# Optimization experiments

Measured on AMD Instinct MI355X. Metric: run time of the kernel, lower is better.

Reference implementation:

```python
import jax, jax.numpy as jnp
import numpy as np

EPS = 1e-10


def setup_inputs() -> dict:
    key = jax.random.key(0)
    k_in, k_len, k_u, k_w, k_b, k_cb = jax.random.split(key, 6)
    B, S, D_in = 16, 4096, 512
    G, C, D_out = 2, 320, 256
    inputs = jax.random.normal(k_in, (B, S, D_in), dtype=jnp.float32)
    valid_lengths = jax.random.randint(k_len, (B,), 1, S + 1, dtype=jnp.int64)
    noise_u = jax.random.uniform(k_u, (B, S, G, C), dtype=jnp.float32)
    # projector params (nn.Linear default init scale is irrelevant for correctness)
    W = jax.random.normal(k_w, (G * C, D_in), dtype=jnp.float32) * (1.0 / np.sqrt(D_in))
    b = jax.random.normal(k_b, (G * C,), dtype=jnp.float32) * 0.01
    codebook = jax.random.uniform(k_cb, (G, C, D_out // G), dtype=jnp.float32,
                                  minval=-1.0 / C, maxval=1.0 / C)
    temperature = jnp.asarray(2.0, dtype=jnp.float32)
    return {"inputs": inputs, "valid_lengths": valid_lengths, "noise_u": noise_u,
            "W": W, "b": b, "codebook": codebook, "temperature": temperature}


def reference(inputs, valid_lengths, noise_u, W, b, codebook, temperature):
    B, S, _ = inputs.shape
    G, C, Dg = codebook.shape
    # dense projector GEMM: [B,S,Din] @ [Din,G*C]
    logits = (jnp.einsum('bsi,oi->bso', inputs, W) + b).reshape(B, S, G, C)
    # gumbel-softmax with straight-through hard selection (F.gumbel_softmax)
    gumbels = -jnp.log(-jnp.log(noise_u + EPS) + EPS)
    y_soft = jax.nn.softmax((logits + gumbels) / temperature, axis=-1)
    idx = jnp.argmax(y_soft, axis=-1)                       # [B,S,G]
    y_hard = jax.nn.one_hot(idx, C, dtype=y_soft.dtype)
    choice_probs = y_hard - jax.lax.stop_gradient(y_soft) + y_soft
    # masked usage stats over valid positions
    soft_probs = jax.nn.softmax(logits, axis=-1)            # [B,S,G,C]
    mask = (jnp.arange(S)[None, :] < valid_lengths[:, None]).astype(soft_probs.dtype)
    masked_sum = jnp.einsum('bsgc,bs->gc', soft_probs, mask)
    usage = masked_sum / jnp.sum(mask)
    # per-group codebook lookup via einsum against small table
    quantized = jnp.einsum('bsgc,gcd->bsgd', choice_probs, codebook).reshape(B, S, G * Dg)
    return quantized, usage
```

## Files before the change

kernel.cpp:

```cpp
#include <hip/hip_runtime.h>
#include <math.h>

#define NB 16
#define NS 4096
#define DIN 512
#define NG 2
#define NC 320
#define GC 640
#define DG 128
#define NROW (NB*NS)
#define EPSV 1e-10f

typedef __attribute__((ext_vector_type(4))) float f32x4;
typedef __attribute__((ext_vector_type(8))) _Float16 f16x8;
typedef __attribute__((ext_vector_type(4))) _Float16 f16x4v;

__device__ __forceinline__ void gload_lds16(const void* g, void* l) {
    __builtin_amdgcn_global_load_lds(
        (const __attribute__((address_space(1))) void*)g,
        (__attribute__((address_space(3))) void*)l,
        16, 0, 0);
}

__global__ __launch_bounds__(256) void cvt_split(
    const float* __restrict__ src, _Float16* __restrict__ h,
    _Float16* __restrict__ l, int n4)
{
    int i = blockIdx.x * 256 + threadIdx.x;
    if (i >= n4) return;
    float4 v = ((const float4*)src)[i];
    f16x4v vh, vl;
    float xs[4] = {v.x, v.y, v.z, v.w};
    #pragma unroll
    for (int j = 0; j < 4; ++j) {
        _Float16 hh = (_Float16)xs[j];
        vh[j] = hh;
        vl[j] = (_Float16)((xs[j] - (float)hh) * 2048.0f);
    }
    ((f16x4v*)h)[i] = vh;
    ((f16x4v*)l)[i] = vl;
}

__global__ __launch_bounds__(256, 2) void mfma_logits(
    const _Float16* __restrict__ Xh, const _Float16* __restrict__ Xl,
    const _Float16* __restrict__ Wh, const _Float16* __restrict__ Wl,
    const float* __restrict__ bias, float* __restrict__ logits)
{
    __shared__ _Float16 sA[2][2][128 * 32];
    __shared__ _Float16 sB[2][2][128 * 32];

    const int t = threadIdx.x;
    const int lane = t & 63;
    const int w = t >> 6;
    const int wm = w >> 1, wn = w & 1;

    const int p = blockIdx.x;
    const int o = (p & 7) * 320 + (p >> 3);
    const int mb = o / 5, nb = o - mb * 5;
    const int row0 = mb * 128, n0 = nb * 128;

    const int rl = lane >> 2;
    const int sl = (lane & 3) ^ ((lane >> 3) & 3);

    auto stage = [&](int b, int k0) {
        #pragma unroll
        for (int j = 0; j < 2; ++j) {
            int i = 2 * w + j;
            int ro = 16 * i + rl;
            size_t ga = (size_t)(row0 + ro) * DIN + k0 + 8 * sl;
            size_t gb = (size_t)(n0 + ro) * DIN + k0 + 8 * sl;
            gload_lds16(Xh + ga, &sA[b][0][i * 512]);
            gload_lds16(Xl + ga, &sA[b][1][i * 512]);
            gload_lds16(Wh + gb, &sB[b][0][i * 512]);
            gload_lds16(Wl + gb, &sB[b][1][i * 512]);
        }
    };

    f32x4 accA[4][4], accB[4][4];
    const f32x4 zz = {0.f, 0.f, 0.f, 0.f};
    #pragma unroll
    for (int mt = 0; mt < 4; ++mt)
        #pragma unroll
        for (int nt = 0; nt < 4; ++nt) { accA[mt][nt] = zz; accB[mt][nt] = zz; }

    stage(0, 0);
    __syncthreads();

    for (int ks = 0; ks < 16; ++ks) {
        const int cur = ks & 1;
        if (ks < 15) stage(cur ^ 1, (ks + 1) * 32);

        f16x8 ah[4], al[4], bh[4], bl[4];
        #pragma unroll
        for (int mt = 0; mt < 4; ++mt) {
            int r = wm * 64 + mt * 16 + (lane & 15);
            int idx = r * 32 + 8 * ((lane >> 4) ^ ((r >> 1) & 3));
            ah[mt] = *(const f16x8*)&sA[cur][0][idx];
            al[mt] = *(const f16x8*)&sA[cur][1][idx];
        }
        #pragma unroll
        for (int nt = 0; nt < 4; ++nt) {
            int r = wn * 64 + nt * 16 + (lane & 15);
            int idx = r * 32 + 8 * ((lane >> 4) ^ ((r >> 1) & 3));
            bh[nt] = *(const f16x8*)&sB[cur][0][idx];
            bl[nt] = *(const f16x8*)&sB[cur][1][idx];
        }
        #pragma unroll
        for (int mt = 0; mt < 4; ++mt)
            #pragma unroll
            for (int nt = 0; nt < 4; ++nt) {
                accA[mt][nt] = __builtin_amdgcn_mfma_f32_16x16x32_f16(ah[mt], bh[nt], accA[mt][nt], 0, 0, 0);
                accB[mt][nt] = __builtin_amdgcn_mfma_f32_16x16x32_f16(ah[mt], bl[nt], accB[mt][nt], 0, 0, 0);
                accB[mt][nt] = __builtin_amdgcn_mfma_f32_16x16x32_f16(al[mt], bh[nt], accB[mt][nt], 0, 0, 0);
            }
        __syncthreads();
    }

    #pragma unroll
    for (int nt = 0; nt < 4; ++nt) {
        int col = n0 + wn * 64 + nt * 16 + (lane & 15);
        float bv = bias[col];
        #pragma unroll
        for (int mt = 0; mt < 4; ++mt) {
            #pragma unroll
            for (int q = 0; q < 4; ++q) {
                int row = row0 + wm * 64 + mt * 16 + (lane >> 4) * 4 + q;
                logits[(size_t)row * GC + col] =
                    accA[mt][nt][q] + accB[mt][nt][q] * (1.0f / 2048.0f) + bv;
            }
        }
    }
}

#define RTB 32
__global__ __launch_bounds__(256, 8) void epilogue(
    const float* __restrict__ logits, const int* __restrict__ vlen,
    const float* __restrict__ U, const float* __restrict__ CB,
    float* __restrict__ out, float* __restrict__ gacc)
{
    __shared__ float uacc[GC];
    const int t = threadIdx.x;
    const int lane = t & 63;
    const int wid = t >> 6;
    const int row0 = blockIdx.x * RTB;

    for (int i = t; i < GC; i += 256) uacc[i] = 0.0f;
    __syncthreads();

    const int vl = vlen[row0 >> 12];

    float ureg[10];
    #pragma unroll
    for (int j = 0; j < 10; ++j) ureg[j] = 0.0f;

    #pragma unroll
    for (int r = 0; r < 8; ++r) {
        const int row = row0 + wid * 8 + r;
        const bool valid = (row & (NS - 1)) < vl;

        float lg[10], zz[10];
        #pragma unroll
        for (int j = 0; j < 10; ++j)
            lg[j] = logits[(size_t)row * GC + lane + 64 * j];
        #pragma unroll
        for (int j = 0; j < 10; ++j) {
            float u = U[(size_t)row * GC + lane + 64 * j];
            zz[j] = lg[j] - logf(-logf(u + EPSV) + EPSV);
        }

        #pragma unroll
        for (int g = 0; g < 2; ++g) {
            const int j0 = g * 5;

            float mv = zz[j0];
            #pragma unroll
            for (int j = j0 + 1; j < j0 + 5; ++j) mv = fmaxf(mv, zz[j]);
            #pragma unroll
            for (int d = 1; d < 64; d <<= 1) mv = fmaxf(mv, __shfl_xor(mv, d));

            int c = 0;
            #pragma unroll
            for (int jj = 4; jj >= 0; --jj) {
                unsigned long long b = __ballot(zz[j0 + jj] == mv);
                if (b) c = (__ffsll(b) - 1) + 64 * jj;
            }

            float pe[5], s2 = 0.0f;
            #pragma unroll
            for (int jj = 0; jj < 5; ++jj) {
                pe[jj] = __expf(lg[j0 + jj]);
                s2 += pe[jj];
            }
            #pragma unroll
            for (int d = 1; d < 64; d <<= 1) s2 += __shfl_xor(s2, d);
            if (valid) {
                const float inv = 1.0f / s2;
                #pragma unroll
                for (int jj = 0; jj < 5; ++jj) ureg[j0 + jj] += pe[jj] * inv;
            }

            const float2 cv = ((const float2*)(CB + ((size_t)g * NC + c) * DG))[lane];
            ((float2*)(out + (size_t)row * (NG * DG) + g * DG))[lane] = cv;
        }
    }

    #pragma unroll
    for (int j = 0; j < 10; ++j)
        atomicAdd(&uacc[lane + 64 * j], ureg[j]);

    __syncthreads();
    for (int i = t; i < GC; i += 256) atomicAdd(&gacc[i], uacc[i]);
}

__global__ void finalize_usage(const float* __restrict__ gacc,
                               const int* __restrict__ vlen,
                               float* __restrict__ usage_out)
{
    int total = 0;
    #pragma unroll
    for (int b = 0; b < NB; ++b) total += vlen[b];
    int o = threadIdx.x;
    if (o < GC) usage_out[o] = gacc[o] / (float)total;
}

#define RT 32
#define KC 8
#define NIT (DIN/KC)

__global__ void transpose_w(const float* __restrict__ W, float* __restrict__ Wt) {
    int idx = blockIdx.x * 256 + threadIdx.x;
    if (idx >= GC * DIN) return;
    int k = idx / GC, o = idx - k * GC;
    Wt[idx] = W[(size_t)o * DIN + k];
}

__global__ __launch_bounds__(256, 2) void fused_main(
    const float* __restrict__ X, const int* __restrict__ vlen,
    const float* __restrict__ U, const float* __restrict__ Wt,
    const float* __restrict__ bias, const float* __restrict__ CB,
    const float* __restrict__ tptr, float* __restrict__ out,
    float* __restrict__ gacc)
{
    __shared__ __align__(16) float WtC[2][KC][GC];
    __shared__ __align__(16) float AC[2][RT][KC];
    __shared__ float uacc[GC];

    const int t = threadIdx.x;
    const int lane = t & 63;
    const int wid = t >> 6;
    const int row0 = blockIdx.x * RT;

    for (int i = t; i < GC; i += 256) uacc[i] = 0.0f;

    float acc[8][10];
    #pragma unroll
    for (int r = 0; r < 8; ++r)
        #pragma unroll
        for (int j = 0; j < 10; ++j) acc[r][j] = 0.0f;

    auto stage = [&](int b, int k0) {
        const float* gw = Wt + (size_t)k0 * GC;
        #pragma unroll
        for (int i = 0; i < 5; ++i) {
            int base = (wid * 5 + i) * 256;
            gload_lds16(gw + base + 4 * lane, &WtC[b][0][0] + base);
        }
        if (wid == 0) {
            const float* gx = X + (size_t)(row0 + (lane >> 1)) * DIN + k0 + 4 * (lane & 1);
            gload_lds16(gx, &AC[b][0][0]);
        }
    };

    stage(0, 0);
    __syncthreads();

    int cur = 0;
    for (int it = 0; it < NIT; ++it) {
        if (it + 1 < NIT) stage(cur ^ 1, (it + 1) * KC);
        #pragma unroll
        for (int kk = 0; kk < KC; ++kk) {
            float w[10];
            #pragma unroll
            for (int j = 0; j < 10; ++j) w[j] = WtC[cur][kk][lane + 64 * j];
            #pragma unroll
            for (int r = 0; r < 8; ++r) {
                float a = AC[cur][wid * 8 + r][kk];
                #pragma unroll
                for (int j = 0; j < 10; ++j) acc[r][j] = fmaf(a, w[j], acc[r][j]);
            }
        }
        __syncthreads();
        cur ^= 1;
    }

    float bv[10];
    #pragma unroll
    for (int j = 0; j < 10; ++j) bv[j] = bias[lane + 64 * j];
    #pragma unroll
    for (int r = 0; r < 8; ++r)
        #pragma unroll
        for (int j = 0; j < 10; ++j) acc[r][j] += bv[j];

    const float T = *tptr;
    const int vl = vlen[row0 >> 12];

    #pragma unroll
    for (int r = 0; r < 8; ++r) {
        const int row = row0 + wid * 8 + r;
        const int ss = row & (NS - 1);
        const bool valid = ss < vl;

        float z[10];
        #pragma unroll
        for (int j = 0; j < 10; ++j) {
            float u = U[(size_t)row * GC + lane + 64 * j];
            float gn = -logf(-logf(u + EPSV) + EPSV);
            z[j] = (acc[r][j] + gn) / T;
        }

        #pragma unroll
        for (int g = 0; g < 2; ++g) {
            const int j0 = g * 5;
            float mv = z[j0];
            int mo = lane + 64 * j0;
            #pragma unroll
            for (int j = j0 + 1; j < j0 + 5; ++j) {
                if (z[j] > mv) { mv = z[j]; mo = lane + 64 * j; }
            }
            #pragma unroll
            for (int d = 1; d < 64; d <<= 1) {
                float ov = __shfl_xor(mv, d);
                int   oo = __shfl_xor(mo, d);
                if (ov > mv || (ov == mv && oo < mo)) { mv = ov; mo = oo; }
            }
            float se = 0.0f;
            #pragma unroll
            for (int j = j0; j < j0 + 5; ++j) se += expf(z[j] - mv);
            #pragma unroll
            for (int d = 1; d < 64; d <<= 1) se += __shfl_xor(se, d);
            float y = 1.0f / se;
            float q = (1.0f - y) + y;

            float m2 = acc[r][j0];
            #pragma unroll
            for (int j = j0 + 1; j < j0 + 5; ++j) m2 = fmaxf(m2, acc[r][j]);
            #pragma unroll
            for (int d = 1; d < 64; d <<= 1) m2 = fmaxf(m2, __shfl_xor(m2, d));
            float pe[5];
            float s2 = 0.0f;
            #pragma unroll
            for (int jj = 0; jj < 5; ++jj) {
                pe[jj] = expf(acc[r][j0 + jj] - m2);
                s2 += pe[jj];
            }
            #pragma unroll
            for (int d = 1; d < 64; d <<= 1) s2 += __shfl_xor(s2, d);
            if (valid) {
                #pragma unroll
                for (int jj = 0; jj < 5; ++jj)
                    atomicAdd(&uacc[lane + 64 * (j0 + jj)], pe[jj] / s2);
            }

            const int c = mo - g * NC;
            const float2 cv = ((const float2*)(CB + ((size_t)g * NC + c) * DG))[lane];
            float2 ov2;
            ov2.x = q * cv.x;
            ov2.y = q * cv.y;
            ((float2*)(out + (size_t)row * (NG * DG) + g * DG))[lane] = ov2;
        }
    }

    __syncthreads();
    for (int i = t; i < GC; i += 256) atomicAdd(&gacc[i], uacc[i]);
}

extern "C" void kernel_launch(void* const* d_in, const int* in_sizes, int n_in,
                              void* d_out, int out_size, void* d_ws, size_t ws_size,
                              hipStream_t stream)
{
    const float* X    = (const float*)d_in[0];
    const int*   vlen = (const int*)d_in[1];
    const float* U    = (const float*)d_in[2];
    const float* W    = (const float*)d_in[3];
    const float* bias = (const float*)d_in[4];
    const float* CB   = (const float*)d_in[5];
    const float* T    = (const float*)d_in[6];
    float* out = (float*)d_out;

    char* ws = (char*)d_ws;
    float*     Wt   = (float*)ws;
    float*     gacc = (float*)(ws + 1310720);
    _Float16*  Whh  = (_Float16*)(ws + 1313792);
    _Float16*  Wll  = (_Float16*)(ws + 1969152);
    _Float16*  Xhh  = (_Float16*)(ws + 2624512);
    _Float16*  Xll  = (_Float16*)(ws + 69733376);
    float*     lgts = (float*)(ws + 136842240);
    const size_t need = 136842240ull + 167772160ull;

    hipMemsetAsync(gacc, 0, GC * sizeof(float), stream);

    if (ws_size >= need) {
        const int nx4 = NROW * DIN / 4;
        const int nw4 = GC * DIN / 4;
        cvt_split<<<(nx4 + 255) / 256, 256, 0, stream>>>(X, Xhh, Xll, nx4);
        cvt_split<<<(nw4 + 255) / 256, 256, 0, stream>>>(W, Whh, Wll, nw4);
        mfma_logits<<<(NROW / 128) * 5, 256, 0, stream>>>(Xhh, Xll, Whh, Wll, bias, lgts);
        epilogue<<<NROW / RTB, 256, 0, stream>>>(lgts, vlen, U, CB, out, gacc);
    } else {
        transpose_w<<<(GC * DIN + 255) / 256, 256, 0, stream>>>(W, Wt);
        fused_main<<<NROW / RT, 256, 0, stream>>>(X, vlen, U, Wt, bias, CB, T, out, gacc);
    }
    finalize_usage<<<1, GC, 0, stream>>>(gacc, vlen, out + (size_t)NROW * (NG * DG));
}
```

Measured before the change: 333.0 us.

## Fuse fp32-to-fp16 split of X into GEMM A-tile staging

Drops the separate cvt_split pass over the large input X. The GEMM kernel now loads fp32 X directly into registers, splits each value into high and low fp16 parts, and writes them to LDS after the MFMAs, overlapping with the next tile's loads. This avoids writing and re-reading two fp16 copies of X, about 128 MB of extra traffic. It also moves to 512-thread blocks with 8 waves, each wave covering a 64x32 output sub-tile, which cuts per-thread accumulator registers. The cost is that the conversion work and register-staged loads now sit inside the GEMM main loop.

```diff
diff --git a/kernel.cpp b/kernel.cpp
--- a/kernel.cpp
+++ b/kernel.cpp
@@ -41,8 +41,8 @@
     ((f16x4v*)l)[i] = vl;
 }
 
-__global__ __launch_bounds__(256, 2) void mfma_logits(
-    const _Float16* __restrict__ Xh, const _Float16* __restrict__ Xl,
+__global__ __launch_bounds__(512, 3) void mfma_logits2(
+    const float* __restrict__ X,
     const _Float16* __restrict__ Wh, const _Float16* __restrict__ Wl,
     const float* __restrict__ bias, float* __restrict__ logits)
 {
@@ -52,7 +52,7 @@
     const int t = threadIdx.x;
     const int lane = t & 63;
     const int w = t >> 6;
-    const int wm = w >> 1, wn = w & 1;
+    const int wm = w >> 2, wn = w & 3;
 
     const int p = blockIdx.x;
     const int o = (p & 7) * 320 + (p >> 3);
@@ -62,35 +62,52 @@
     const int rl = lane >> 2;
     const int sl = (lane & 3) ^ ((lane >> 3) & 3);
 
-    auto stage = [&](int b, int k0) {
-        #pragma unroll
-        for (int j = 0; j < 2; ++j) {
-            int i = 2 * w + j;
-            int ro = 16 * i + rl;
-            size_t ga = (size_t)(row0 + ro) * DIN + k0 + 8 * sl;
-            size_t gb = (size_t)(n0 + ro) * DIN + k0 + 8 * sl;
-            gload_lds16(Xh + ga, &sA[b][0][i * 512]);
-            gload_lds16(Xl + ga, &sA[b][1][i * 512]);
-            gload_lds16(Wh + gb, &sB[b][0][i * 512]);
-            gload_lds16(Wl + gb, &sB[b][1][i * 512]);
-        }
+    auto stageB = [&](int b, int k0) {
+        int ro = 16 * w + rl;
+        size_t gb = (size_t)(n0 + ro) * DIN + k0 + 8 * sl;
+        gload_lds16(Wh + gb, &sB[b][0][w * 512]);
+        gload_lds16(Wl + gb, &sB[b][1][w * 512]);
     };
 
-    f32x4 accA[4][4], accB[4][4];
+    const int ar = t >> 2, aq = t & 3;
+    const int aidx = ar * 32 + 8 * (aq ^ ((ar >> 1) & 3));
+    const float* aga = X + (size_t)(row0 + ar) * DIN + 8 * aq;
+
+    float4 a0, a1;
+    auto loadA = [&](int k0) {
+        a0 = ((const float4*)(aga + k0))[0];
+        a1 = ((const float4*)(aga + k0))[1];
+    };
+    auto writeA = [&](int b) {
+        float xs[8] = {a0.x, a0.y, a0.z, a0.w, a1.x, a1.y, a1.z, a1.w};
+        f16x8 h, l;
+        #pragma unroll
+        for (int j = 0; j < 8; ++j) {
+            _Float16 hh = (_Float16)xs[j];
+            h[j] = hh;
+            l[j] = (_Float16)((xs[j] - (float)hh) * 2048.0f);
+        }
+        *(f16x8*)&sA[b][0][aidx] = h;
+        *(f16x8*)&sA[b][1][aidx] = l;
+    };
+
+    f32x4 accA[4][2], accB[4][2];
     const f32x4 zz = {0.f, 0.f, 0.f, 0.f};
     #pragma unroll
     for (int mt = 0; mt < 4; ++mt)
         #pragma unroll
-        for (int nt = 0; nt < 4; ++nt) { accA[mt][nt] = zz; accB[mt][nt] = zz; }
-
-    stage(0, 0);
+        for (int nt = 0; nt < 2; ++nt) { accA[mt][nt] = zz; accB[mt][nt] = zz; }
+
+    loadA(0);
+    stageB(0, 0);
+    writeA(0);
     __syncthreads();
 
     for (int ks = 0; ks < 16; ++ks) {
         const int cur = ks & 1;
-        if (ks < 15) stage(cur ^ 1, (ks + 1) * 32);
-
-        f16x8 ah[4], al[4], bh[4], bl[4];
+        if (ks < 15) { loadA((ks + 1) * 32); stageB(cur ^ 1, (ks + 1) * 32); }
+
+        f16x8 ah[4], al[4], bh[2], bl[2];
         #pragma unroll
         for (int mt = 0; mt < 4; ++mt) {
             int r = wm * 64 + mt * 16 + (lane & 15);
@@ -99,8 +116,8 @@
             al[mt] = *(const f16x8*)&sA[cur][1][idx];
         }
         #pragma unroll
-        for (int nt = 0; nt < 4; ++nt) {
-            int r = wn * 64 + nt * 16 + (lane & 15);
+        for (int nt = 0; nt < 2; ++nt) {
+            int r = wn * 32 + nt * 16 + (lane & 15);
             int idx = r * 32 + 8 * ((lane >> 4) ^ ((r >> 1) & 3));
             bh[nt] = *(const f16x8*)&sB[cur][0][idx];
             bl[nt] = *(const f16x8*)&sB[cur][1][idx];
@@ -108,17 +125,19 @@
         #pragma unroll
         for (int mt = 0; mt < 4; ++mt)
             #pragma unroll
-            for (int nt = 0; nt < 4; ++nt) {
+            for (int nt = 0; nt < 2; ++nt) {
                 accA[mt][nt] = __builtin_amdgcn_mfma_f32_16x16x32_f16(ah[mt], bh[nt], accA[mt][nt], 0, 0, 0);
                 accB[mt][nt] = __builtin_amdgcn_mfma_f32_16x16x32_f16(ah[mt], bl[nt], accB[mt][nt], 0, 0, 0);
                 accB[mt][nt] = __builtin_amdgcn_mfma_f32_16x16x32_f16(al[mt], bh[nt], accB[mt][nt], 0, 0, 0);
             }
+
+        if (ks < 15) writeA(cur ^ 1);
         __syncthreads();
     }
 
     #pragma unroll
-    for (int nt = 0; nt < 4; ++nt) {
-        int col = n0 + wn * 64 + nt * 16 + (lane & 15);
+    for (int nt = 0; nt < 2; ++nt) {
+        int col = n0 + wn * 32 + nt * 16 + (lane & 15);
         float bv = bias[col];
         #pragma unroll
         for (int mt = 0; mt < 4; ++mt) {
@@ -388,23 +407,19 @@
     float* out = (float*)d_out;
 
     char* ws = (char*)d_ws;
-    float*     Wt   = (float*)ws;
-    float*     gacc = (float*)(ws + 1310720);
-    _Float16*  Whh  = (_Float16*)(ws + 1313792);
-    _Float16*  Wll  = (_Float16*)(ws + 1969152);
-    _Float16*  Xhh  = (_Float16*)(ws + 2624512);
-    _Float16*  Xll  = (_Float16*)(ws + 69733376);
-    float*     lgts = (float*)(ws + 136842240);
-    const size_t need = 136842240ull + 167772160ull;
+    float*     gacc = (float*)ws;
+    _Float16*  Whh  = (_Float16*)(ws + 4096);
+    _Float16*  Wll  = (_Float16*)(ws + 659456);
+    float*     lgts = (float*)(ws + 1314816);
+    float*     Wt   = (float*)(ws + 4096);
+    const size_t need = 1314816ull + 167772160ull;
 
     hipMemsetAsync(gacc, 0, GC * sizeof(float), stream);
 
     if (ws_size >= need) {
-        const int nx4 = NROW * DIN / 4;
         const int nw4 = GC * DIN / 4;
-        cvt_split<<<(nx4 + 255) / 256, 256, 0, stream>>>(X, Xhh, Xll, nx4);
         cvt_split<<<(nw4 + 255) / 256, 256, 0, stream>>>(W, Whh, Wll, nw4);
-        mfma_logits<<<(NROW / 128) * 5, 256, 0, stream>>>(Xhh, Xll, Whh, Wll, bias, lgts);
+        mfma_logits2<<<(NROW / 128) * 5, 512, 0, stream>>>(X, Whh, Wll, bias, lgts);
         epilogue<<<NROW / RTB, 256, 0, stream>>>(lgts, vlen, U, CB, out, gacc);
     } else {
         transpose_w<<<(GC * DIN + 255) / 256, 256, 0, stream>>>(W, Wt);
```

Result: faster. 269.0 us (-19.2%).
